# Optimization experiments

Measured on AMD Instinct MI355X. Metric: run time of the kernel, lower is better.

The kernel has to match this reference:

```python
import jax, jax.numpy as jnp
import numpy as np

B, C, H, W = 8, 8, 512, 512

# one-pixel shifts with zero padding (equivalent to the bmm with shift matrices)
def shift_right(x):  # out[..., c] = x[..., c-1]
    return jnp.pad(x, ((0, 0), (0, 0), (1, 0)))[:, :, :-1]
def shift_left(x):   # out[..., c] = x[..., c+1]
    return jnp.pad(x, ((0, 0), (0, 0), (0, 1)))[:, :, 1:]
def shift_up(x):     # out[r] = x[r+1]
    return jnp.pad(x, ((0, 0), (0, 1), (0, 0)))[:, 1:, :]
def shift_down(x):   # out[r] = x[r-1]
    return jnp.pad(x, ((0, 0), (1, 0), (0, 0)))[:, :-1, :]

def bilater_voting(c):
    # c: [B, 8, H, W] probabilities
    right        = shift_right(c[:, 4])
    left         = shift_left(c[:, 3])
    left_bottom  = shift_left(shift_down(c[:, 5]))
    right_above  = shift_right(shift_up(c[:, 2]))
    left_above   = shift_left(shift_up(c[:, 0]))
    bottom       = shift_down(c[:, 6])
    up           = shift_up(c[:, 1])
    right_bottom = shift_right(shift_down(c[:, 7]))
    a1 = c[:, 3] * right
    a2 = c[:, 4] * left
    a3 = c[:, 1] * bottom
    a4 = c[:, 6] * up
    a5 = c[:, 2] * left_bottom
    a6 = c[:, 5] * right_above
    a7 = c[:, 0] * right_bottom
    a8 = c[:, 7] * left_above
    vote_out = jnp.stack([a7, a3, a5, a1, a2, a6, a4, a8], axis=1)
    glo_map = jnp.mean(vote_out, axis=1)
    return glo_map, vote_out

def bce(p, t):
    # matches torch F.binary_cross_entropy (mean reduction, log clamped at -100)
    logp = jnp.clip(jnp.log(p), -100.0, None)
    log1mp = jnp.clip(jnp.log(1.0 - p), -100.0, None)
    return -jnp.mean(t * logp + (1.0 - t) * log1mp)

def setup_inputs() -> dict:
    key = jax.random.key(0)
    k1, k2, k3, k4 = jax.random.split(key, 4)
    atts = jax.random.normal(k1, (B, C, H, W), dtype=jnp.float32)
    dets = jax.random.normal(k2, (B, C, H, W), dtype=jnp.float32)
    target = jax.random.randint(k3, (B, 1, H, W), 0, 2).astype(jnp.float32)
    con_target = jax.random.randint(k4, (B, C, H, W), 0, 2).astype(jnp.float32)
    return {"atts": atts, "dets": dets, "target": target, "con_target": con_target}

def reference(atts, dets, target, con_target):
    # edge mask from connectivity GT: pixels with 0 < sum < 8
    sum_conn = jnp.sum(con_target, axis=1)  # [B, H, W]
    edge_conn = jnp.where((sum_conn < 8.0) & (sum_conn > 0.0), 1.0, 0.0)

    atts_p = jax.nn.sigmoid(atts)
    dets_p = jax.nn.sigmoid(dets)

    glo_map1, vote_out1 = bilater_voting(atts_p)
    glo_map2, vote_out2 = bilater_voting(dets_p)

    # edge/decouple loss on dets branch
    pred_mask_min = 1.0 - jnp.min(vote_out2, axis=1)
    pred_mask_min = pred_mask_min * edge_conn
    decouple_map = glo_map2 * (1.0 - edge_conn) + pred_mask_min
    de_loss2 = bce(decouple_map[:, None], target)

    bce_loss1 = bce(glo_map1[:, None], target)
    bicon_loss1 = bce(vote_out1, con_target)
    conn_loss1 = bce(atts_p, con_target)
    bicon_loss2 = bce(vote_out2, con_target)
    conn_loss2 = bce(dets_p, con_target)

    loss = (0.2 * bicon_loss1 + 0.8 * conn_loss1 + bce_loss1
            + 0.2 * bicon_loss2 + 0.8 * conn_loss2 + de_loss2)
    return loss
```

## Files before the change

### kernel.cpp

```cpp
#include <hip/hip_runtime.h>

#define BB 8
#define CC 8
#define HH 512
#define WW 512
#define HWSZ (HH * WW)

typedef float v4 __attribute__((ext_vector_type(4)));

#define LOG2_CLAMP -144.26950409f

__device__ __forceinline__ v4 uload4(const float* __restrict__ p) {
    v4 r;
    __builtin_memcpy(&r, p, sizeof(v4));
    return r;
}
__device__ __forceinline__ v4 aload4(const float* __restrict__ p) {
    return *(const v4* __restrict__)p;
}

__device__ __forceinline__ v4 sig4(v4 x) {
    v4 r;
#pragma unroll
    for (int i = 0; i < 4; ++i)
        r[i] = __builtin_amdgcn_rcpf(1.0f + __expf(-x[i]));
    return r;
}

__device__ __forceinline__ v4 vsel(v4 t, v4 x, v4 y) {
    v4 r;
#pragma unroll
    for (int i = 0; i < 4; ++i) r[i] = (t[i] > 0.5f) ? x[i] : y[i];
    return r;
}

template <bool NEED_MIN>
__device__ __forceinline__ void eval_branch(
    const v4* __restrict__ cr, const v4* __restrict__ nr,
    const v4* __restrict__ cv, const v4* __restrict__ mk,
    v4& glo, v4& vmin, float& Lbic, float& Lcon)
{
    v4 pb0 = {1.f, 1.f, 1.f, 1.f}, pb1 = {1.f, 1.f, 1.f, 1.f};
    v4 pc  = {1.f, 1.f, 1.f, 1.f};
    v4 vsum = {0.f, 0.f, 0.f, 0.f};
    if (NEED_MIN) vmin = {1e30f, 1e30f, 1e30f, 1e30f};
    v4 one = {1.f, 1.f, 1.f, 1.f};

#pragma unroll
    for (int k = 0; k < 8; ++k) {
        v4 s = sig4(cr[k]);
        v4 n = sig4(nr[k]) * mk[k];
        v4 v = s * n;
        vsum += v;
        if (NEED_MIN) vmin = __builtin_elementwise_min(vmin, v);
        v4 t  = cv[k];
        v4 av = vsel(t, v, one - v);
        v4 as = vsel(t, s, one - s);
        if (k < 4) pb0 *= av; else pb1 *= av;
        pc *= as;
    }
    glo = vsum * 0.125f;

    float lb = 0.f, lc = 0.f;
#pragma unroll
    for (int i = 0; i < 4; ++i) {
        lb += fmaxf(__log2f(pb0[i]), LOG2_CLAMP) + fmaxf(__log2f(pb1[i]), LOG2_CLAMP);
        lc += fmaxf(__log2f(pc[i]), LOG2_CLAMP);
    }
    Lbic = lb;
    Lcon = lc;
}

__global__ __launch_bounds__(256, 2) void bicon_loss_kernel(
    const float* __restrict__ atts, const float* __restrict__ dets,
    const float* __restrict__ target, const float* __restrict__ con,
    float* __restrict__ out)
{
    const int idx = blockIdx.x * 256 + threadIdx.x;
    const int w0  = (idx & 127) << 2;
    const int row = idx >> 7;
    const int h   = row & (HH - 1);
    const int b   = row >> 9;

    const int hm = (h > 0) ? h - 1 : 0;
    const int hp = (h < HH - 1) ? h + 1 : HH - 1;
    const float mh0 = (h > 0) ? 1.0f : 0.0f;
    const float mh1 = (h < HH - 1) ? 1.0f : 0.0f;
    const v4 mwL = {(w0 == 0) ? 0.0f : 1.0f, 1.f, 1.f, 1.f};
    const v4 mwR = {1.f, 1.f, 1.f, (w0 == WW - 4) ? 0.0f : 1.0f};

    const int offC = h * WW + w0;
    const int offU = hm * WW + w0;
    const int offD = hp * WW + w0;

    const float* __restrict__ ab = atts + b * CC * HWSZ;
    const float* __restrict__ db = dets + b * CC * HWSZ;
    const float* __restrict__ cb = con  + b * CC * HWSZ;

    v4 ac[8], an[8], dc[8], dn[8], cv[8], t4;
#pragma unroll
    for (int c = 0; c < 8; ++c) ac[c] = aload4(ab + c * HWSZ + offC);
    an[0] = uload4(ab + 7 * HWSZ + offU - 1);
    an[1] = aload4(ab + 6 * HWSZ + offU);
    an[2] = uload4(ab + 5 * HWSZ + offU + 1);
    an[3] = uload4(ab + 4 * HWSZ + offC - 1);
    an[4] = uload4(ab + 3 * HWSZ + offC + 1);
    an[5] = uload4(ab + 2 * HWSZ + offD - 1);
    an[6] = aload4(ab + 1 * HWSZ + offD);
    an[7] = uload4(ab + 0 * HWSZ + offD + 1);
#pragma unroll
    for (int c = 0; c < 8; ++c) dc[c] = aload4(db + c * HWSZ + offC);
    dn[0] = uload4(db + 7 * HWSZ + offU - 1);
    dn[1] = aload4(db + 6 * HWSZ + offU);
    dn[2] = uload4(db + 5 * HWSZ + offU + 1);
    dn[3] = uload4(db + 4 * HWSZ + offC - 1);
    dn[4] = uload4(db + 3 * HWSZ + offC + 1);
    dn[5] = uload4(db + 2 * HWSZ + offD - 1);
    dn[6] = aload4(db + 1 * HWSZ + offD);
    dn[7] = uload4(db + 0 * HWSZ + offD + 1);
#pragma unroll
    for (int c = 0; c < 8; ++c) cv[c] = aload4(cb + c * HWSZ + offC);
    t4 = aload4(target + b * HWSZ + offC);

    v4 mk[8];
    mk[0] = mwL * mh0;
    mk[1] = {mh0, mh0, mh0, mh0};
    mk[2] = mwR * mh0;
    mk[3] = mwL;
    mk[4] = mwR;
    mk[5] = mwL * mh1;
    mk[6] = {mh1, mh1, mh1, mh1};
    mk[7] = mwR * mh1;

    v4 csum = {0.f, 0.f, 0.f, 0.f};
#pragma unroll
    for (int c = 0; c < 8; ++c) csum += cv[c];
    v4 edge;
#pragma unroll
    for (int i = 0; i < 4; ++i)
        edge[i] = (csum[i] < 8.0f && csum[i] > 0.0f) ? 1.0f : 0.0f;

    v4 glo1, glo2, vmin1, vmin2;
    float Lb1, Lc1, Lb2, Lc2;
    eval_branch<false>(ac, an, cv, mk, glo1, vmin1, Lb1, Lc1);
    eval_branch<true >(dc, dn, cv, mk, glo2, vmin2, Lb2, Lc2);

    float Lp = 0.f;
#pragma unroll
    for (int i = 0; i < 4; ++i) {
        float dec = (edge[i] > 0.5f) ? (1.0f - vmin2[i]) : glo2[i];
        float a  = (t4[i] > 0.5f) ? glo1[i] : 1.0f - glo1[i];
        float bs = (t4[i] > 0.5f) ? dec     : 1.0f - dec;
        Lp += fmaxf(__log2f(a * bs), LOG2_CLAMP);
    }

    const float wbic = 0.2f / (float)(BB * CC * HWSZ);
    const float wcon = 0.8f / (float)(BB * CC * HWSZ);
    const float wpix = 1.0f / (float)(BB * HWSZ);
    const float ln2  = 0.69314718056f;

    float local = -(wbic * (Lb1 + Lb2) + wcon * (Lc1 + Lc2) + wpix * Lp) * ln2;

#pragma unroll
    for (int off = 32; off > 0; off >>= 1)
        local += __shfl_down(local, off, 64);

    __shared__ float wsum[4];
    const int lane = threadIdx.x & 63;
    const int wid  = threadIdx.x >> 6;
    if (lane == 0) wsum[wid] = local;
    __syncthreads();
    if (threadIdx.x == 0) {
        float s = wsum[0] + wsum[1] + wsum[2] + wsum[3];
        atomicAdd(out, s);
    }
}

extern "C" void kernel_launch(void* const* d_in, const int* in_sizes, int n_in,
                              void* d_out, int out_size, void* d_ws, size_t ws_size,
                              hipStream_t stream) {
    const float* atts   = (const float*)d_in[0];
    const float* dets   = (const float*)d_in[1];
    const float* target = (const float*)d_in[2];
    const float* con    = (const float*)d_in[3];
    float* out = (float*)d_out;

    hipMemsetAsync(out, 0, sizeof(float), stream);

    const int ngroups = BB * HH * WW / 4;
    bicon_loss_kernel<<<ngroups / 256, 256, 0, stream>>>(atts, dets, target, con, out);
}
```

Baseline: 201.0 us.

## Stream atts neighbor loads into LDS and pack connectivity bits to cut registers

Loads the eight shifted atts neighbor vectors with global_load_lds straight into shared memory rather than into registers. Packs the connectivity and target values into bitmasks, replaces per-lane mask vectors with scalar masks, and computes the dets branch first while the LDS loads are in flight. Also remaps block indices across groups of eight and raises launch bounds to 4 blocks per SIMD. The aim is lower register pressure and higher occupancy for this memory-bound kernel, at the cost of 32 KB of LDS per block and a manual vmcnt wait.

Measured after the change: 208.8 us. 3.9% more time.

```diff
diff --git a/kernel.cpp b/kernel.cpp
--- a/kernel.cpp
+++ b/kernel.cpp
@@ -1,4 +1,5 @@
 #include <hip/hip_runtime.h>
+#include <stdint.h>
 
 #define BB 8
 #define CC 8
@@ -27,67 +28,37 @@
     return r;
 }
 
-__device__ __forceinline__ v4 vsel(v4 t, v4 x, v4 y) {
-    v4 r;
-#pragma unroll
-    for (int i = 0; i < 4; ++i) r[i] = (t[i] > 0.5f) ? x[i] : y[i];
-    return r;
-}
-
-template <bool NEED_MIN>
-__device__ __forceinline__ void eval_branch(
-    const v4* __restrict__ cr, const v4* __restrict__ nr,
-    const v4* __restrict__ cv, const v4* __restrict__ mk,
-    v4& glo, v4& vmin, float& Lbic, float& Lcon)
-{
-    v4 pb0 = {1.f, 1.f, 1.f, 1.f}, pb1 = {1.f, 1.f, 1.f, 1.f};
-    v4 pc  = {1.f, 1.f, 1.f, 1.f};
-    v4 vsum = {0.f, 0.f, 0.f, 0.f};
-    if (NEED_MIN) vmin = {1e30f, 1e30f, 1e30f, 1e30f};
-    v4 one = {1.f, 1.f, 1.f, 1.f};
-
-#pragma unroll
-    for (int k = 0; k < 8; ++k) {
-        v4 s = sig4(cr[k]);
-        v4 n = sig4(nr[k]) * mk[k];
-        v4 v = s * n;
-        vsum += v;
-        if (NEED_MIN) vmin = __builtin_elementwise_min(vmin, v);
-        v4 t  = cv[k];
-        v4 av = vsel(t, v, one - v);
-        v4 as = vsel(t, s, one - s);
-        if (k < 4) pb0 *= av; else pb1 *= av;
-        pc *= as;
-    }
-    glo = vsum * 0.125f;
-
-    float lb = 0.f, lc = 0.f;
-#pragma unroll
-    for (int i = 0; i < 4; ++i) {
-        lb += fmaxf(__log2f(pb0[i]), LOG2_CLAMP) + fmaxf(__log2f(pb1[i]), LOG2_CLAMP);
-        lc += fmaxf(__log2f(pc[i]), LOG2_CLAMP);
-    }
-    Lbic = lb;
-    Lcon = lc;
-}
-
-__global__ __launch_bounds__(256, 2) void bicon_loss_kernel(
+__device__ __forceinline__ void gload_lds16(const float* g, float* l) {
+    __builtin_amdgcn_global_load_lds(
+        (const __attribute__((address_space(1))) void*)g,
+        (__attribute__((address_space(3))) void*)l, 16, 0, 0);
+}
+
+__global__ __launch_bounds__(256, 4) void bicon_loss_kernel(
     const float* __restrict__ atts, const float* __restrict__ dets,
     const float* __restrict__ target, const float* __restrict__ con,
     float* __restrict__ out)
 {
-    const int idx = blockIdx.x * 256 + threadIdx.x;
-    const int w0  = (idx & 127) << 2;
-    const int row = idx >> 7;
-    const int h   = row & (HH - 1);
-    const int b   = row >> 9;
+    __shared__ __align__(16) float an_lds[8][4][256];
+
+    const int nchunk = (int)gridDim.x >> 3;
+    const int bid = ((int)blockIdx.x & 7) * nchunk + ((int)blockIdx.x >> 3);
+
+    const int tid  = (int)threadIdx.x;
+    const int idx  = bid * 256 + tid;
+    const int w0   = (idx & 127) << 2;
+    const int row  = idx >> 7;
+    const int h    = row & (HH - 1);
+    const int b    = row >> 9;
+    const int lane = tid & 63;
+    const int wid  = tid >> 6;
 
     const int hm = (h > 0) ? h - 1 : 0;
     const int hp = (h < HH - 1) ? h + 1 : HH - 1;
     const float mh0 = (h > 0) ? 1.0f : 0.0f;
     const float mh1 = (h < HH - 1) ? 1.0f : 0.0f;
-    const v4 mwL = {(w0 == 0) ? 0.0f : 1.0f, 1.f, 1.f, 1.f};
-    const v4 mwR = {1.f, 1.f, 1.f, (w0 == WW - 4) ? 0.0f : 1.0f};
+    const float mw0 = (w0 == 0) ? 0.0f : 1.0f;
+    const float mw3 = (w0 == WW - 4) ? 0.0f : 1.0f;
 
     const int offC = h * WW + w0;
     const int offU = hm * WW + w0;
@@ -97,17 +68,16 @@
     const float* __restrict__ db = dets + b * CC * HWSZ;
     const float* __restrict__ cb = con  + b * CC * HWSZ;
 
-    v4 ac[8], an[8], dc[8], dn[8], cv[8], t4;
-#pragma unroll
-    for (int c = 0; c < 8; ++c) ac[c] = aload4(ab + c * HWSZ + offC);
-    an[0] = uload4(ab + 7 * HWSZ + offU - 1);
-    an[1] = aload4(ab + 6 * HWSZ + offU);
-    an[2] = uload4(ab + 5 * HWSZ + offU + 1);
-    an[3] = uload4(ab + 4 * HWSZ + offC - 1);
-    an[4] = uload4(ab + 3 * HWSZ + offC + 1);
-    an[5] = uload4(ab + 2 * HWSZ + offD - 1);
-    an[6] = aload4(ab + 1 * HWSZ + offD);
-    an[7] = uload4(ab + 0 * HWSZ + offD + 1);
+    gload_lds16(ab + 7 * HWSZ + offU - 1, &an_lds[0][wid][0]);
+    gload_lds16(ab + 6 * HWSZ + offU    , &an_lds[1][wid][0]);
+    gload_lds16(ab + 5 * HWSZ + offU + 1, &an_lds[2][wid][0]);
+    gload_lds16(ab + 4 * HWSZ + offC - 1, &an_lds[3][wid][0]);
+    gload_lds16(ab + 3 * HWSZ + offC + 1, &an_lds[4][wid][0]);
+    gload_lds16(ab + 2 * HWSZ + offD - 1, &an_lds[5][wid][0]);
+    gload_lds16(ab + 1 * HWSZ + offD    , &an_lds[6][wid][0]);
+    gload_lds16(ab + 0 * HWSZ + offD + 1, &an_lds[7][wid][0]);
+
+    v4 dc[8], dn[8], ac[8];
 #pragma unroll
     for (int c = 0; c < 8; ++c) dc[c] = aload4(db + c * HWSZ + offC);
     dn[0] = uload4(db + 7 * HWSZ + offU - 1);
@@ -119,38 +89,97 @@
     dn[6] = aload4(db + 1 * HWSZ + offD);
     dn[7] = uload4(db + 0 * HWSZ + offD + 1);
 #pragma unroll
-    for (int c = 0; c < 8; ++c) cv[c] = aload4(cb + c * HWSZ + offC);
-    t4 = aload4(target + b * HWSZ + offC);
-
-    v4 mk[8];
-    mk[0] = mwL * mh0;
-    mk[1] = {mh0, mh0, mh0, mh0};
-    mk[2] = mwR * mh0;
-    mk[3] = mwL;
-    mk[4] = mwR;
-    mk[5] = mwL * mh1;
-    mk[6] = {mh1, mh1, mh1, mh1};
-    mk[7] = mwR * mh1;
-
-    v4 csum = {0.f, 0.f, 0.f, 0.f};
-#pragma unroll
-    for (int c = 0; c < 8; ++c) csum += cv[c];
-    v4 edge;
+    for (int c = 0; c < 8; ++c) ac[c] = aload4(ab + c * HWSZ + offC);
+
+    uint32_t sel = 0u;
+#pragma unroll
+    for (int c = 0; c < 8; ++c) {
+        v4 cvv = aload4(cb + c * HWSZ + offC);
+#pragma unroll
+        for (int i = 0; i < 4; ++i)
+            if (cvv[i] > 0.5f) sel |= (1u << (c * 4 + i));
+    }
+    v4 tv = aload4(target + b * HWSZ + offC);
+    uint32_t tb = 0u;
 #pragma unroll
     for (int i = 0; i < 4; ++i)
-        edge[i] = (csum[i] < 8.0f && csum[i] > 0.0f) ? 1.0f : 0.0f;
-
-    v4 glo1, glo2, vmin1, vmin2;
-    float Lb1, Lc1, Lb2, Lc2;
-    eval_branch<false>(ac, an, cv, mk, glo1, vmin1, Lb1, Lc1);
-    eval_branch<true >(dc, dn, cv, mk, glo2, vmin2, Lb2, Lc2);
+        if (tv[i] > 0.5f) tb |= (1u << i);
+
+    const float mkA[8] = {mh0 * mw0, mh0, mh0,       mw0, 1.f, mh1 * mw0, mh1, mh1};
+    const float mkB[8] = {mh0,       mh0, mh0,       1.f, 1.f, mh1,       mh1, mh1};
+    const float mkC[8] = {mh0,       mh0, mh0 * mw3, 1.f, mw3, mh1,       mh1, mh1 * mw3};
+
+    const v4 one = {1.f, 1.f, 1.f, 1.f};
+
+    v4 pb0 = one, pb1 = one, pc = one;
+    v4 vsum = {0.f, 0.f, 0.f, 0.f};
+    v4 vmin = {1e30f, 1e30f, 1e30f, 1e30f};
+#pragma unroll
+    for (int k = 0; k < 8; ++k) {
+        v4 s = sig4(dc[k]);
+        v4 n = sig4(dn[k]);
+        n[0] *= mkA[k]; n[1] *= mkB[k]; n[2] *= mkB[k]; n[3] *= mkC[k];
+        v4 v = s * n;
+        vsum += v;
+        vmin = __builtin_elementwise_min(vmin, v);
+        v4 av, as;
+#pragma unroll
+        for (int i = 0; i < 4; ++i) {
+            const bool bt = (sel >> (k * 4 + i)) & 1u;
+            av[i] = bt ? v[i] : 1.0f - v[i];
+            as[i] = bt ? s[i] : 1.0f - s[i];
+        }
+        if (k < 4) pb0 *= av; else pb1 *= av;
+        pc *= as;
+    }
+    const v4 glo2  = vsum * 0.125f;
+    const v4 vmin2 = vmin;
+    float Lb2 = 0.f, Lc2 = 0.f;
+#pragma unroll
+    for (int i = 0; i < 4; ++i) {
+        Lb2 += fmaxf(__log2f(pb0[i]), LOG2_CLAMP) + fmaxf(__log2f(pb1[i]), LOG2_CLAMP);
+        Lc2 += fmaxf(__log2f(pc[i]), LOG2_CLAMP);
+    }
+
+    asm volatile("s_waitcnt vmcnt(0)" ::: "memory");
+
+    v4 qb0 = one, qb1 = one, qc = one;
+    v4 qsum = {0.f, 0.f, 0.f, 0.f};
+#pragma unroll
+    for (int k = 0; k < 8; ++k) {
+        v4 s = sig4(ac[k]);
+        v4 n = sig4(*(const v4*)&an_lds[k][wid][lane * 4]);
+        n[0] *= mkA[k]; n[1] *= mkB[k]; n[2] *= mkB[k]; n[3] *= mkC[k];
+        v4 v = s * n;
+        qsum += v;
+        v4 av, as;
+#pragma unroll
+        for (int i = 0; i < 4; ++i) {
+            const bool bt = (sel >> (k * 4 + i)) & 1u;
+            av[i] = bt ? v[i] : 1.0f - v[i];
+            as[i] = bt ? s[i] : 1.0f - s[i];
+        }
+        if (k < 4) qb0 *= av; else qb1 *= av;
+        qc *= as;
+    }
+    const v4 glo1 = qsum * 0.125f;
+    float Lb1 = 0.f, Lc1 = 0.f;
+#pragma unroll
+    for (int i = 0; i < 4; ++i) {
+        Lb1 += fmaxf(__log2f(qb0[i]), LOG2_CLAMP) + fmaxf(__log2f(qb1[i]), LOG2_CLAMP);
+        Lc1 += fmaxf(__log2f(qc[i]), LOG2_CLAMP);
+    }
 
     float Lp = 0.f;
 #pragma unroll
     for (int i = 0; i < 4; ++i) {
-        float dec = (edge[i] > 0.5f) ? (1.0f - vmin2[i]) : glo2[i];
-        float a  = (t4[i] > 0.5f) ? glo1[i] : 1.0f - glo1[i];
-        float bs = (t4[i] > 0.5f) ? dec     : 1.0f - dec;
+        const uint32_t mI    = 0x11111111u << i;
+        const uint32_t bitsI = sel & mI;
+        const bool edge = (bitsI != 0u) && (bitsI != mI);
+        const float dec = edge ? (1.0f - vmin2[i]) : glo2[i];
+        const bool  ti  = (tb >> i) & 1u;
+        const float a   = ti ? glo1[i] : 1.0f - glo1[i];
+        const float bs  = ti ? dec     : 1.0f - dec;
         Lp += fmaxf(__log2f(a * bs), LOG2_CLAMP);
     }
 
@@ -166,13 +195,10 @@
         local += __shfl_down(local, off, 64);
 
     __shared__ float wsum[4];
-    const int lane = threadIdx.x & 63;
-    const int wid  = threadIdx.x >> 6;
     if (lane == 0) wsum[wid] = local;
     __syncthreads();
-    if (threadIdx.x == 0) {
-        float s = wsum[0] + wsum[1] + wsum[2] + wsum[3];
-        atomicAdd(out, s);
+    if (tid == 0) {
+        atomicAdd(out, wsum[0] + wsum[1] + wsum[2] + wsum[3]);
     }
 }
 
```

## Pack connectivity targets into bitmask, raise occupancy, and remap block order

Applied to the files above, without the earlier changes.

Turns the eight connectivity vectors and the target into 32-bit and 4-bit masks right after loading, so those registers are freed before the dets loads. Border masks become scalar per-lane factors instead of vectors, and the edge test is computed from the bitmask. Launch bounds rise from 2 to 4 blocks per SIMD to allow higher occupancy. Block indices are permuted across 8 interleaved chunks to change the DRAM/XCD access pattern. The higher occupancy target may force register spills.

Measured after the change: 251.6 us. 25.2% more time.

```diff
diff --git a/kernel.cpp b/kernel.cpp
--- a/kernel.cpp
+++ b/kernel.cpp
@@ -1,4 +1,5 @@
 #include <hip/hip_runtime.h>
+#include <stdint.h>
 
 #define BB 8
 #define CC 8
@@ -27,35 +28,33 @@
     return r;
 }
 
-__device__ __forceinline__ v4 vsel(v4 t, v4 x, v4 y) {
-    v4 r;
-#pragma unroll
-    for (int i = 0; i < 4; ++i) r[i] = (t[i] > 0.5f) ? x[i] : y[i];
-    return r;
-}
-
 template <bool NEED_MIN>
 __device__ __forceinline__ void eval_branch(
-    const v4* __restrict__ cr, const v4* __restrict__ nr,
-    const v4* __restrict__ cv, const v4* __restrict__ mk,
+    const v4* __restrict__ cr, const v4* __restrict__ nr, uint32_t sel,
+    const float* __restrict__ mkA, const float* __restrict__ mkB,
+    const float* __restrict__ mkC,
     v4& glo, v4& vmin, float& Lbic, float& Lcon)
 {
-    v4 pb0 = {1.f, 1.f, 1.f, 1.f}, pb1 = {1.f, 1.f, 1.f, 1.f};
-    v4 pc  = {1.f, 1.f, 1.f, 1.f};
+    const v4 one = {1.f, 1.f, 1.f, 1.f};
+    v4 pb0 = one, pb1 = one, pc = one;
     v4 vsum = {0.f, 0.f, 0.f, 0.f};
     if (NEED_MIN) vmin = {1e30f, 1e30f, 1e30f, 1e30f};
-    v4 one = {1.f, 1.f, 1.f, 1.f};
 
 #pragma unroll
     for (int k = 0; k < 8; ++k) {
         v4 s = sig4(cr[k]);
-        v4 n = sig4(nr[k]) * mk[k];
+        v4 n = sig4(nr[k]);
+        n[0] *= mkA[k]; n[1] *= mkB[k]; n[2] *= mkB[k]; n[3] *= mkC[k];
         v4 v = s * n;
         vsum += v;
         if (NEED_MIN) vmin = __builtin_elementwise_min(vmin, v);
-        v4 t  = cv[k];
-        v4 av = vsel(t, v, one - v);
-        v4 as = vsel(t, s, one - s);
+        v4 av, as;
+#pragma unroll
+        for (int i = 0; i < 4; ++i) {
+            const bool bt = (sel >> (k * 4 + i)) & 1u;
+            av[i] = bt ? v[i] : 1.0f - v[i];
+            as[i] = bt ? s[i] : 1.0f - s[i];
+        }
         if (k < 4) pb0 *= av; else pb1 *= av;
         pc *= as;
     }
@@ -71,12 +70,15 @@
     Lcon = lc;
 }
 
-__global__ __launch_bounds__(256, 2) void bicon_loss_kernel(
+__global__ __launch_bounds__(256, 4) void bicon_loss_kernel(
     const float* __restrict__ atts, const float* __restrict__ dets,
     const float* __restrict__ target, const float* __restrict__ con,
     float* __restrict__ out)
 {
-    const int idx = blockIdx.x * 256 + threadIdx.x;
+    const int nchunk = (int)gridDim.x >> 3;
+    const int bid = ((int)blockIdx.x & 7) * nchunk + ((int)blockIdx.x >> 3);
+
+    const int idx = bid * 256 + (int)threadIdx.x;
     const int w0  = (idx & 127) << 2;
     const int row = idx >> 7;
     const int h   = row & (HH - 1);
@@ -86,8 +88,8 @@
     const int hp = (h < HH - 1) ? h + 1 : HH - 1;
     const float mh0 = (h > 0) ? 1.0f : 0.0f;
     const float mh1 = (h < HH - 1) ? 1.0f : 0.0f;
-    const v4 mwL = {(w0 == 0) ? 0.0f : 1.0f, 1.f, 1.f, 1.f};
-    const v4 mwR = {1.f, 1.f, 1.f, (w0 == WW - 4) ? 0.0f : 1.0f};
+    const float mw0 = (w0 == 0) ? 0.0f : 1.0f;
+    const float mw3 = (w0 == WW - 4) ? 0.0f : 1.0f;
 
     const int offC = h * WW + w0;
     const int offU = hm * WW + w0;
@@ -97,7 +99,12 @@
     const float* __restrict__ db = dets + b * CC * HWSZ;
     const float* __restrict__ cb = con  + b * CC * HWSZ;
 
-    v4 ac[8], an[8], dc[8], dn[8], cv[8], t4;
+    v4 cvv[8];
+#pragma unroll
+    for (int c = 0; c < 8; ++c) cvv[c] = aload4(cb + c * HWSZ + offC);
+    v4 tv = aload4(target + b * HWSZ + offC);
+
+    v4 ac[8], an[8];
 #pragma unroll
     for (int c = 0; c < 8; ++c) ac[c] = aload4(ab + c * HWSZ + offC);
     an[0] = uload4(ab + 7 * HWSZ + offU - 1);
@@ -108,6 +115,19 @@
     an[5] = uload4(ab + 2 * HWSZ + offD - 1);
     an[6] = aload4(ab + 1 * HWSZ + offD);
     an[7] = uload4(ab + 0 * HWSZ + offD + 1);
+
+    uint32_t sel = 0u;
+#pragma unroll
+    for (int c = 0; c < 8; ++c)
+#pragma unroll
+        for (int i = 0; i < 4; ++i)
+            if (cvv[c][i] > 0.5f) sel |= (1u << (c * 4 + i));
+    uint32_t tb = 0u;
+#pragma unroll
+    for (int i = 0; i < 4; ++i)
+        if (tv[i] > 0.5f) tb |= (1u << i);
+
+    v4 dc[8], dn[8];
 #pragma unroll
     for (int c = 0; c < 8; ++c) dc[c] = aload4(db + c * HWSZ + offC);
     dn[0] = uload4(db + 7 * HWSZ + offU - 1);
@@ -118,39 +138,26 @@
     dn[5] = uload4(db + 2 * HWSZ + offD - 1);
     dn[6] = aload4(db + 1 * HWSZ + offD);
     dn[7] = uload4(db + 0 * HWSZ + offD + 1);
-#pragma unroll
-    for (int c = 0; c < 8; ++c) cv[c] = aload4(cb + c * HWSZ + offC);
-    t4 = aload4(target + b * HWSZ + offC);
 
-    v4 mk[8];
-    mk[0] = mwL * mh0;
-    mk[1] = {mh0, mh0, mh0, mh0};
-    mk[2] = mwR * mh0;
-    mk[3] = mwL;
-    mk[4] = mwR;
-    mk[5] = mwL * mh1;
-    mk[6] = {mh1, mh1, mh1, mh1};
-    mk[7] = mwR * mh1;
-
-    v4 csum = {0.f, 0.f, 0.f, 0.f};
-#pragma unroll
-    for (int c = 0; c < 8; ++c) csum += cv[c];
-    v4 edge;
-#pragma unroll
-    for (int i = 0; i < 4; ++i)
-        edge[i] = (csum[i] < 8.0f && csum[i] > 0.0f) ? 1.0f : 0.0f;
+    const float mkA[8] = {mh0 * mw0, mh0, mh0,       mw0, 1.f, mh1 * mw0, mh1, mh1};
+    const float mkB[8] = {mh0,       mh0, mh0,       1.f, 1.f, mh1,       mh1, mh1};
+    const float mkC[8] = {mh0,       mh0, mh0 * mw3, 1.f, mw3, mh1,       mh1, mh1 * mw3};
 
     v4 glo1, glo2, vmin1, vmin2;
     float Lb1, Lc1, Lb2, Lc2;
-    eval_branch<false>(ac, an, cv, mk, glo1, vmin1, Lb1, Lc1);
-    eval_branch<true >(dc, dn, cv, mk, glo2, vmin2, Lb2, Lc2);
+    eval_branch<false>(ac, an, sel, mkA, mkB, mkC, glo1, vmin1, Lb1, Lc1);
+    eval_branch<true >(dc, dn, sel, mkA, mkB, mkC, glo2, vmin2, Lb2, Lc2);
 
     float Lp = 0.f;
 #pragma unroll
     for (int i = 0; i < 4; ++i) {
-        float dec = (edge[i] > 0.5f) ? (1.0f - vmin2[i]) : glo2[i];
-        float a  = (t4[i] > 0.5f) ? glo1[i] : 1.0f - glo1[i];
-        float bs = (t4[i] > 0.5f) ? dec     : 1.0f - dec;
+        const uint32_t mI    = 0x11111111u << i;
+        const uint32_t bitsI = sel & mI;
+        const bool edge = (bitsI != 0u) && (bitsI != mI);
+        const float dec = edge ? (1.0f - vmin2[i]) : glo2[i];
+        const bool  ti  = (tb >> i) & 1u;
+        const float a   = ti ? glo1[i] : 1.0f - glo1[i];
+        const float bs  = ti ? dec     : 1.0f - dec;
         Lp += fmaxf(__log2f(a * bs), LOG2_CLAMP);
     }
 
@@ -171,8 +178,7 @@
     if (lane == 0) wsum[wid] = local;
     __syncthreads();
     if (threadIdx.x == 0) {
-        float s = wsum[0] + wsum[1] + wsum[2] + wsum[3];
-        atomicAdd(out, s);
+        atomicAdd(out, wsum[0] + wsum[1] + wsum[2] + wsum[3]);
     }
 }
 
```
